# Kernel tuning notes

Measured on AMD Instinct MI355X. Metric: run time of the kernel, lower is better.

Reference implementation:

```python
import jax, jax.numpy as jnp
import numpy as np

N_NODES = 100000

def _sage_conv(x, edge_index, W_l, b_l, W_r):
    # PyG SAGEConv default: mean-aggregate neighbor (source) features at dst,
    # then out = lin_l(agg) + lin_r(x). lin_l has bias, lin_r does not.
    src, dst = edge_index[0], edge_index[1]
    msg = x[src]                                   # [E, F]
    summed = jax.ops.segment_sum(msg, dst, num_segments=N_NODES)  # [N, F]
    cnt = jax.ops.segment_sum(jnp.ones((src.shape[0],), x.dtype), dst,
                              num_segments=N_NODES)
    agg = summed / jnp.maximum(cnt, 1.0)[:, None]
    return agg @ W_l + b_l + x @ W_r


def setup_inputs() -> dict:
    key = jax.random.key(0)
    ks = jax.random.split(key, 10)
    F_IN, H, C = 128, 16, 8
    E = 3200000
    x = jax.random.normal(ks[0], (N_NODES, F_IN), dtype=jnp.float32)
    edge_index = jax.random.randint(ks[1], (2, E), 0, N_NODES, dtype=jnp.int64)
    s1 = 1.0 / np.sqrt(F_IN)
    s2 = 1.0 / np.sqrt(H)
    sc = 1.0 / np.sqrt(2 * H)
    return {
        "x": x,
        "edge_index": edge_index,
        "W1_l": jax.random.uniform(ks[2], (F_IN, H), jnp.float32, -s1, s1),
        "b1": jnp.zeros((H,), jnp.float32),
        "W1_r": jax.random.uniform(ks[3], (F_IN, H), jnp.float32, -s1, s1),
        "W2_l": jax.random.uniform(ks[4], (H, H), jnp.float32, -s2, s2),
        "b2": jnp.zeros((H,), jnp.float32),
        "W2_r": jax.random.uniform(ks[5], (H, H), jnp.float32, -s2, s2),
        "Wc": jax.random.uniform(ks[6], (2 * H, C), jnp.float32, -sc, sc),
        "bc": jax.random.uniform(ks[7], (C,), jnp.float32, -sc, sc),
    }


def reference(x, edge_index, W1_l, b1, W1_r, W2_l, b2, W2_r, Wc, bc):
    h = jax.nn.relu(_sage_conv(x, edge_index, W1_l, b1, W1_r))
    # F.dropout(training=False) in eval mode -> identity
    h = jax.nn.relu(_sage_conv(h, edge_index, W2_l, b2, W2_r))
    edge_feat = jnp.concatenate([h[edge_index[0]], h[edge_index[1]]], axis=-1)  # [E, 32]
    logits = edge_feat @ Wc + bc                                                # [E, C]
    return jax.nn.log_softmax(logits, axis=1)
```

## Files before the change

kernel.cpp:

```cpp
#include <hip/hip_runtime.h>
#include <hip/hip_bf16.h>
#include <hip/hip_fp16.h>


#define NBLK 512
#define BUCKET_BITS 9
#define BUCKET_SZ 512
#define MAXNB 256
#define STAGE_CAP 36000

struct __align__(16) H8 { __half2 a, b, c, d; };

__global__ __launch_bounds__(512) void prep_kernel(const int* __restrict__ ei,
                                                   int* __restrict__ counts,
                                                   const float* __restrict__ x,
                                                   const float* __restrict__ W1l,
                                                   const float* __restrict__ W1r,
                                                   __half* __restrict__ yh,
                                                   float* __restrict__ z,
                                                   int E, int N, int NB, int chunk,
                                                   int nbin) {
  __shared__ float smem[64 * 129 + 128 * 32];
  int t = threadIdx.x;
  if ((int)blockIdx.x < nbin) {
    int* hist = (int*)smem;
    for (int i = t; i < NB; i += 512) hist[i] = 0;
    __syncthreads();
    int s = blockIdx.x * chunk;
    int eend = s + chunk; if (eend > E) eend = E;
    for (int e = s + t; e < eend; e += 512)
      atomicAdd(&hist[ei[E + e] >> BUCKET_BITS], 1);
    __syncthreads();
    for (int b = t; b < NB; b += 512)
      counts[b * NBLK + blockIdx.x] = hist[b];
  } else {
    float* Xs = smem;
    float* Ws = smem + 64 * 129;
    int nb = ((int)blockIdx.x - nbin) * 64;
    for (int i = t; i < 128 * 16; i += 512) {
      int kk = i >> 4, c = i & 15;
      Ws[kk * 32 + c] = W1l[i];
      Ws[kk * 32 + 16 + c] = W1r[i];
    }
    const float4* xg = (const float4*)(x + (size_t)nb * 128);
    for (int i4 = t; i4 < 64 * 32; i4 += 512) {
      int r = i4 >> 5, c4 = (i4 & 31) * 4;
      float4 val = make_float4(0.f, 0.f, 0.f, 0.f);
      if (nb + r < N) val = xg[i4];
      float* dp = &Xs[r * 129 + c4];
      dp[0] = val.x; dp[1] = val.y; dp[2] = val.z; dp[3] = val.w;
    }
    __syncthreads();
    int n = t & 63, cg = t >> 6;
    float a0 = 0.f, a1 = 0.f, a2 = 0.f, a3 = 0.f;
    for (int kk = 0; kk < 128; ++kk) {
      float xv = Xs[n * 129 + kk];
      const float* wr = &Ws[kk * 32 + cg * 4];
      a0 += xv * wr[0]; a1 += xv * wr[1]; a2 += xv * wr[2]; a3 += xv * wr[3];
    }
    int node = nb + n;
    if (node < N) {
      int c = cg * 4;
      if (c < 16) {
        __half2* yp = (__half2*)(yh + (size_t)node * 16 + c);
        yp[0] = __floats2half2_rn(a0, a1);
        yp[1] = __floats2half2_rn(a2, a3);
      } else {
        float* op = z + (size_t)node * 16 + (c - 16);
        op[0] = a0; op[1] = a1; op[2] = a2; op[3] = a3;
      }
    }
  }
}

__global__ __launch_bounds__(512) void scan1_kernel(const int* __restrict__ counts,
                                                    int* __restrict__ locoff,
                                                    int* __restrict__ total) {
  __shared__ int wsum[8];
  int b = blockIdx.x;
  int t = threadIdx.x;
  int lane = t & 63, wid = t >> 6;
  int v = counts[b * NBLK + t];
  int incl = v;
#pragma unroll
  for (int d = 1; d < 64; d <<= 1) {
    int u = __shfl_up(incl, d);
    if (lane >= d) incl += u;
  }
  if (lane == 63) wsum[wid] = incl;
  __syncthreads();
  if (t < 64) {
    int w = (t < 8) ? wsum[t] : 0;
#pragma unroll
    for (int d = 1; d < 8; d <<= 1) {
      int u = __shfl_up(w, d);
      if (lane >= d) w += u;
    }
    if (t < 8) wsum[t] = w;
  }
  __syncthreads();
  int excl = ((wid > 0) ? wsum[wid - 1] : 0) + (incl - v);
  locoff[b * NBLK + t] = excl;
  if (t == NBLK - 1) total[b] = excl + v;
}

__global__ __launch_bounds__(512) void binwrite_kernel(const int* __restrict__ ei,
                                                       const int* __restrict__ locoff,
                                                       const int* __restrict__ total,
                                                       int* __restrict__ elist,
                                                       int E, int NB, int chunk) {
  __shared__ int cur[MAXNB];
  __shared__ int ws4[4];
  int t = threadIdx.x;
  int lane = t & 63, wid = t >> 6;
  int v = (t < 256 && t < NB) ? total[t] : 0;
  int incl = v;
#pragma unroll
  for (int d = 1; d < 64; d <<= 1) {
    int u = __shfl_up(incl, d);
    if (lane >= d) incl += u;
  }
  if (t < 256 && lane == 63) ws4[wid] = incl;
  __syncthreads();
  if (t < 64) {
    int w = (t < 4) ? ws4[t] : 0;
#pragma unroll
    for (int d = 1; d < 4; d <<= 1) {
      int u = __shfl_up(w, d);
      if (lane >= d) w += u;
    }
    if (t < 4) ws4[t] = w;
  }
  __syncthreads();
  if (t < 256 && t < NB)
    cur[t] = ((wid > 0) ? ws4[wid - 1] : 0) + (incl - v) + locoff[t * NBLK + blockIdx.x];
  __syncthreads();
  int s = blockIdx.x * chunk;
  int eend = s + chunk; if (eend > E) eend = E;
  for (int e = s + t; e < eend; e += 512) {
    int src = ei[e];
    int dst = ei[E + e];
    int b = dst >> BUCKET_BITS;
    int pos = atomicAdd(&cur[b], 1);
    elist[pos] = ((dst & (BUCKET_SZ - 1)) << 17) | src;
  }
}

__global__ __launch_bounds__(1024) void sort_kernel(int* __restrict__ elist,
                                                    const int* __restrict__ total,
                                                    int* __restrict__ row_csr,
                                                    int N, int NB) {
  extern __shared__ int sm[];
  int* stage = sm;
  int* hist  = sm + STAGE_CAP;
  int* wtmp  = hist + 512;
  __shared__ int beg_s;
  int t = threadIdx.x;
  int b = blockIdx.x;
  int lane = t & 63, wid = t >> 6;
  {
    int v = (t < 256 && t < NB) ? total[t] : 0;
    int incl = v;
#pragma unroll
    for (int d = 1; d < 64; d <<= 1) {
      int u = __shfl_up(incl, d);
      if (lane >= d) incl += u;
    }
    if (t < 256 && lane == 63) wtmp[wid] = incl;
    __syncthreads();
    if (t < 64) {
      int w = (t < 4) ? wtmp[t] : 0;
#pragma unroll
      for (int d = 1; d < 4; d <<= 1) {
        int u = __shfl_up(w, d);
        if (lane >= d) w += u;
      }
      if (t < 4) wtmp[t] = w;
    }
    __syncthreads();
    if (t == b) beg_s = ((wid > 0) ? wtmp[wid - 1] : 0) + (incl - v);
    __syncthreads();
  }
  int beg = beg_s;
  int cnt = total[b];
  if (cnt > STAGE_CAP) cnt = STAGE_CAP;
  for (int i = t; i < cnt; i += 1024) stage[i] = elist[beg + i];
  if (t < 512) hist[t] = 0;
  __syncthreads();
  for (int i = t; i < cnt; i += 1024)
    atomicAdd(&hist[((unsigned)stage[i]) >> 17], 1);
  __syncthreads();
  int v = (t < 512) ? hist[t] : 0;
  int incl = v;
#pragma unroll
  for (int d = 1; d < 64; d <<= 1) {
    int u = __shfl_up(incl, d);
    if (lane >= d) incl += u;
  }
  if (t < 512 && lane == 63) wtmp[wid] = incl;
  __syncthreads();
  if (t < 64) {
    int w = (t < 8) ? wtmp[t] : 0;
#pragma unroll
    for (int d = 1; d < 8; d <<= 1) {
      int u = __shfl_up(w, d);
      if (lane >= d) w += u;
    }
    if (t < 8) wtmp[t] = w;
  }
  __syncthreads();
  if (t < 512) {
    int excl = ((wid > 0) ? wtmp[wid - 1] : 0) + (incl - v);
    hist[t] = excl;
    int node = (b << BUCKET_BITS) + t;
    if (node <= N) row_csr[node] = beg + excl;
  }
  __syncthreads();
  for (int i = t; i < cnt; i += 1024) {
    unsigned ent = (unsigned)stage[i];
    int pos = atomicAdd(&hist[ent >> 17], 1);
    elist[beg + pos] = ent & 0x1FFFF;
  }
}

__global__ __launch_bounds__(256) void agg1_kernel(const __half* __restrict__ yh,
                                                   const float* __restrict__ z,
                                                   const int* __restrict__ row_csr,
                                                   const int* __restrict__ srclist,
                                                   const float* __restrict__ b1,
                                                   const float* __restrict__ W2l,
                                                   const float* __restrict__ W2r,
                                                   __half* __restrict__ ph,
                                                   float* __restrict__ q, int N) {
  __shared__ float Wl_s[256], Wr_s[256], b_s[16];
  int t = threadIdx.x;
  if (t < 256) { Wl_s[t] = W2l[t]; Wr_s[t] = W2r[t]; }
  if (t < 16) b_s[t] = b1[t];
  __syncthreads();
  int g = (blockIdx.x * 256 + t) >> 3;
  int k = t & 7;
  if (g >= N) return;
  int beg = row_csr[g], end = row_csr[g + 1];
  const __half2* yh2 = (const __half2*)yh;
  float a0 = 0.f, a1 = 0.f;
  int j = beg;
  for (; j + 4 <= end; j += 4) {
    int s0 = srclist[j], s1 = srclist[j + 1];
    int s2 = srclist[j + 2], s3 = srclist[j + 3];
    float2 v0 = __half22float2(yh2[(size_t)s0 * 8 + k]);
    float2 v1 = __half22float2(yh2[(size_t)s1 * 8 + k]);
    float2 v2 = __half22float2(yh2[(size_t)s2 * 8 + k]);
    float2 v3 = __half22float2(yh2[(size_t)s3 * 8 + k]);
    a0 += v0.x + v1.x + v2.x + v3.x;
    a1 += v0.y + v1.y + v2.y + v3.y;
  }
  for (; j < end; ++j) {
    float2 v = __half22float2(yh2[(size_t)srclist[j] * 8 + k]);
    a0 += v.x; a1 += v.y;
  }
  int deg = end - beg;
  float inv = 1.f / (float)(deg > 0 ? deg : 1);
  float2 zv = ((const float2*)z)[(size_t)g * 8 + k];
  float h0 = fmaxf(a0 * inv + b_s[2 * k]     + zv.x, 0.f);
  float h1 = fmaxf(a1 * inv + b_s[2 * k + 1] + zv.y, 0.f);
  float pa0 = 0.f, pa1 = 0.f, qa0 = 0.f, qa1 = 0.f;
  int c0 = 2 * k;
#pragma unroll
  for (int kk2 = 0; kk2 < 8; ++kk2) {
    float ha = __shfl(h0, kk2, 8);
    float hb = __shfl(h1, kk2, 8);
    int r0 = 2 * kk2 * 16, r1 = r0 + 16;
    pa0 += ha * Wl_s[r0 + c0]     + hb * Wl_s[r1 + c0];
    pa1 += ha * Wl_s[r0 + c0 + 1] + hb * Wl_s[r1 + c0 + 1];
    qa0 += ha * Wr_s[r0 + c0]     + hb * Wr_s[r1 + c0];
    qa1 += ha * Wr_s[r0 + c0 + 1] + hb * Wr_s[r1 + c0 + 1];
  }
  ((__half2*)ph)[(size_t)g * 8 + k] = __floats2half2_rn(pa0, pa1);
  ((float2*)q)[(size_t)g * 8 + k] = make_float2(qa0, qa1);
}

__global__ __launch_bounds__(256) void agg2_kernel(const __half* __restrict__ ph,
                                                   const float* __restrict__ q,
                                                   const int* __restrict__ row_csr,
                                                   const int* __restrict__ srclist,
                                                   const float* __restrict__ b2,
                                                   const float* __restrict__ Wc,
                                                   __half* __restrict__ Uh,
                                                   __half* __restrict__ Vh, int N) {
  __shared__ float Wc_s[256], b_s[16];
  int t = threadIdx.x;
  if (t < 256) Wc_s[t] = Wc[t];
  if (t < 16) b_s[t] = b2[t];
  __syncthreads();
  int g = (blockIdx.x * 256 + t) >> 3;
  int k = t & 7;
  if (g >= N) return;
  int beg = row_csr[g], end = row_csr[g + 1];
  const __half2* ph2 = (const __half2*)ph;
  float a0 = 0.f, a1 = 0.f;
  int j = beg;
  for (; j + 4 <= end; j += 4) {
    int s0 = srclist[j], s1 = srclist[j + 1];
    int s2 = srclist[j + 2], s3 = srclist[j + 3];
    float2 v0 = __half22float2(ph2[(size_t)s0 * 8 + k]);
    float2 v1 = __half22float2(ph2[(size_t)s1 * 8 + k]);
    float2 v2 = __half22float2(ph2[(size_t)s2 * 8 + k]);
    float2 v3 = __half22float2(ph2[(size_t)s3 * 8 + k]);
    a0 += v0.x + v1.x + v2.x + v3.x;
    a1 += v0.y + v1.y + v2.y + v3.y;
  }
  for (; j < end; ++j) {
    float2 v = __half22float2(ph2[(size_t)srclist[j] * 8 + k]);
    a0 += v.x; a1 += v.y;
  }
  int deg = end - beg;
  float inv = 1.f / (float)(deg > 0 ? deg : 1);
  float2 qv = ((const float2*)q)[(size_t)g * 8 + k];
  float h0 = fmaxf(a0 * inv + b_s[2 * k]     + qv.x, 0.f);
  float h1 = fmaxf(a1 * inv + b_s[2 * k + 1] + qv.y, 0.f);
  int wb = (k < 4) ? 0 : 128;
  int c0 = 2 * (k & 3);
  float o0 = 0.f, o1 = 0.f;
#pragma unroll
  for (int kk2 = 0; kk2 < 8; ++kk2) {
    float ha = __shfl(h0, kk2, 8);
    float hb = __shfl(h1, kk2, 8);
    int r0 = wb + 2 * kk2 * 8, r1 = r0 + 8;
    o0 += ha * Wc_s[r0 + c0]     + hb * Wc_s[r1 + c0];
    o1 += ha * Wc_s[r0 + c0 + 1] + hb * Wc_s[r1 + c0 + 1];
  }
  __half2 o = __floats2half2_rn(o0, o1);
  if (k < 4) ((__half2*)Uh)[(size_t)g * 4 + k] = o;
  else       ((__half2*)Vh)[(size_t)g * 4 + (k - 4)] = o;
}

__global__ __launch_bounds__(256) void edge_out_kernel(const int* __restrict__ ei,
                                                       const __half* __restrict__ Uh,
                                                       const __half* __restrict__ Vh,
                                                       const float* __restrict__ bc,
                                                       float* __restrict__ out, int E) {
  int base = blockIdx.x * 1024 + threadIdx.x;
  float4 c0 = ((const float4*)bc)[0], c1 = ((const float4*)bc)[1];
  int s[4], d[4];
#pragma unroll
  for (int ii = 0; ii < 4; ++ii) {
    int e = base + ii * 256;
    s[ii] = (e < E) ? ei[e] : 0;
    d[ii] = (e < E) ? ei[E + e] : 0;
  }
  H8 u8[4], v8[4];
#pragma unroll
  for (int ii = 0; ii < 4; ++ii) {
    u8[ii] = *(const H8*)(Uh + (size_t)s[ii] * 8);
    v8[ii] = *(const H8*)(Vh + (size_t)d[ii] * 8);
  }
#pragma unroll
  for (int ii = 0; ii < 4; ++ii) {
    int e = base + ii * 256;
    if (e >= E) continue;
    float2 ua = __half22float2(u8[ii].a), ub = __half22float2(u8[ii].b);
    float2 uc = __half22float2(u8[ii].c), ud = __half22float2(u8[ii].d);
    float2 va = __half22float2(v8[ii].a), vb = __half22float2(v8[ii].b);
    float2 vc = __half22float2(v8[ii].c), vd = __half22float2(v8[ii].d);
    float tv[8];
    tv[0] = ua.x + va.x + c0.x; tv[1] = ua.y + va.y + c0.y;
    tv[2] = ub.x + vb.x + c0.z; tv[3] = ub.y + vb.y + c0.w;
    tv[4] = uc.x + vc.x + c1.x; tv[5] = uc.y + vc.y + c1.y;
    tv[6] = ud.x + vd.x + c1.z; tv[7] = ud.y + vd.y + c1.w;
    float m = tv[0];
#pragma unroll
    for (int c = 1; c < 8; ++c) m = fmaxf(m, tv[c]);
    float ssum = 0.f;
#pragma unroll
    for (int c = 0; c < 8; ++c) ssum += __expf(tv[c] - m);
    float lse = m + __logf(ssum);
    float4 o0 = make_float4(tv[0] - lse, tv[1] - lse, tv[2] - lse, tv[3] - lse);
    float4 o1 = make_float4(tv[4] - lse, tv[5] - lse, tv[6] - lse, tv[7] - lse);
    float4* op = (float4*)(out + (size_t)e * 8);
    op[0] = o0; op[1] = o1;
  }
}

extern "C" void kernel_launch(void* const* d_in, const int* in_sizes, int n_in,
                              void* d_out, int out_size, void* d_ws, size_t ws_size,
                              hipStream_t stream) {
  const float* x   = (const float*)d_in[0];
  const int*   ei  = (const int*)d_in[1];
  const float* W1l = (const float*)d_in[2];
  const float* b1  = (const float*)d_in[3];
  const float* W1r = (const float*)d_in[4];
  const float* W2l = (const float*)d_in[5];
  const float* b2  = (const float*)d_in[6];
  const float* W2r = (const float*)d_in[7];
  const float* Wc  = (const float*)d_in[8];
  const float* bc  = (const float*)d_in[9];
  float* out = (float*)d_out;

  const int N = in_sizes[0] / 128;
  const int E = in_sizes[1] / 2;
  const size_t N16 = (size_t)N * 16;
  const int NB = (N + BUCKET_SZ - 1) >> BUCKET_BITS;
  const int chunk = (E + NBLK - 1) / NBLK;

  __half* yh = (__half*)d_ws;
  __half* ph = yh + N16;
  __half* Uh = ph + N16;
  __half* Vh = Uh + (size_t)N * 8;
  float*  z  = (float*)(Vh + (size_t)N * 8);
  float*  q  = z + N16;
  int* counts  = (int*)(q + N16);
  int* locoff  = counts + NB * NBLK;
  int* total   = locoff + NB * NBLK;
  int* elist   = total + NB;
  int* row_csr = elist + E;

  int lin1_blocks = (N + 63) / 64;
  prep_kernel<<<NBLK + lin1_blocks, 512, 0, stream>>>(ei, counts, x, W1l, W1r,
                                                      yh, z, E, N, NB, chunk, NBLK);
  scan1_kernel<<<NB, 512, 0, stream>>>(counts, locoff, total);
  binwrite_kernel<<<NBLK, 512, 0, stream>>>(ei, locoff, total, elist, E, NB, chunk);
  size_t smem = (STAGE_CAP + 512 + 16) * sizeof(int);
  sort_kernel<<<NB, 1024, smem, stream>>>(elist, total, row_csr, N, NB);

  int ngrid = (N * 8 + 255) / 256;
  agg1_kernel<<<ngrid, 256, 0, stream>>>(yh, z, row_csr, elist, b1, W2l, W2r, ph, q, N);
  agg2_kernel<<<ngrid, 256, 0, stream>>>(ph, q, row_csr, elist, b2, Wc, Uh, Vh, N);

  int egrid = (E + 1023) / 1024;
  edge_out_kernel<<<egrid, 256, 0, stream>>>(ei, Uh, Vh, bc, out, E);
}
```

Baseline: 197.2 us.

## Fuse first-layer aggregation into bucket sort kernel using LDS-resident sorted lists

Merges agg1 into the bucket sort kernel. Each sort block keeps its sorted source list in shared memory and aggregates its 512 destination nodes right away, then applies the second-layer weights. This removes a kernel launch and the global re-read of row_csr and srclist. In exchange, the gather phase runs on only about 196 large blocks instead of thousands of small ones, and shared memory use per block grows. STAGE_CAP is halved so the staging and sorted buffers both fit, and edge_out now uses nontemporal loads for the edge indices.

```diff
diff --git a/kernel.cpp b/kernel.cpp
--- a/kernel.cpp
+++ b/kernel.cpp
@@ -7,7 +7,7 @@
 #define BUCKET_BITS 9
 #define BUCKET_SZ 512
 #define MAXNB 256
-#define STAGE_CAP 36000
+#define STAGE_CAP 18000
 
 struct __align__(16) H8 { __half2 a, b, c, d; };
 
@@ -146,18 +146,31 @@
   }
 }
 
-__global__ __launch_bounds__(1024) void sort_kernel(int* __restrict__ elist,
-                                                    const int* __restrict__ total,
-                                                    int* __restrict__ row_csr,
-                                                    int N, int NB) {
+__global__ __launch_bounds__(1024) void sortagg_kernel(int* __restrict__ elist,
+                                                       const int* __restrict__ total,
+                                                       int* __restrict__ row_csr,
+                                                       const __half* __restrict__ yh,
+                                                       const float* __restrict__ z,
+                                                       const float* __restrict__ b1,
+                                                       const float* __restrict__ W2l,
+                                                       const float* __restrict__ W2r,
+                                                       __half* __restrict__ ph,
+                                                       float* __restrict__ q,
+                                                       int N, int NB) {
   extern __shared__ int sm[];
-  int* stage = sm;
-  int* hist  = sm + STAGE_CAP;
-  int* wtmp  = hist + 512;
+  int* stage  = sm;
+  int* sorted = sm + STAGE_CAP;
+  int* hist   = sm + 2 * STAGE_CAP;
+  int* wtmp   = hist + 512;
+  float* Wl_s = (float*)(wtmp + 16);
+  float* Wr_s = Wl_s + 256;
+  float* b_s  = Wr_s + 256;
   __shared__ int beg_s;
   int t = threadIdx.x;
   int b = blockIdx.x;
   int lane = t & 63, wid = t >> 6;
+  if (t < 256) { Wl_s[t] = W2l[t]; Wr_s[t] = W2r[t]; }
+  else if (t < 272) b_s[t - 256] = b1[t - 256];
   {
     int v = (t < 256 && t < NB) ? total[t] : 0;
     int incl = v;
@@ -190,93 +203,89 @@
   for (int i = t; i < cnt; i += 1024)
     atomicAdd(&hist[((unsigned)stage[i]) >> 17], 1);
   __syncthreads();
-  int v = (t < 512) ? hist[t] : 0;
-  int incl = v;
-#pragma unroll
-  for (int d = 1; d < 64; d <<= 1) {
-    int u = __shfl_up(incl, d);
-    if (lane >= d) incl += u;
-  }
-  if (t < 512 && lane == 63) wtmp[wid] = incl;
-  __syncthreads();
-  if (t < 64) {
-    int w = (t < 8) ? wtmp[t] : 0;
-#pragma unroll
-    for (int d = 1; d < 8; d <<= 1) {
-      int u = __shfl_up(w, d);
-      if (lane >= d) w += u;
-    }
-    if (t < 8) wtmp[t] = w;
-  }
-  __syncthreads();
-  if (t < 512) {
-    int excl = ((wid > 0) ? wtmp[wid - 1] : 0) + (incl - v);
-    hist[t] = excl;
-    int node = (b << BUCKET_BITS) + t;
-    if (node <= N) row_csr[node] = beg + excl;
+  {
+    int v = (t < 512) ? hist[t] : 0;
+    int incl = v;
+#pragma unroll
+    for (int d = 1; d < 64; d <<= 1) {
+      int u = __shfl_up(incl, d);
+      if (lane >= d) incl += u;
+    }
+    if (t < 512 && lane == 63) wtmp[wid] = incl;
+    __syncthreads();
+    if (t < 64) {
+      int w = (t < 8) ? wtmp[t] : 0;
+#pragma unroll
+      for (int d = 1; d < 8; d <<= 1) {
+        int u = __shfl_up(w, d);
+        if (lane >= d) w += u;
+      }
+      if (t < 8) wtmp[t] = w;
+    }
+    __syncthreads();
+    if (t < 512) {
+      int excl = ((wid > 0) ? wtmp[wid - 1] : 0) + (incl - v);
+      hist[t] = excl;
+      int node = (b << BUCKET_BITS) + t;
+      if (node <= N) row_csr[node] = beg + excl;
+    }
   }
   __syncthreads();
   for (int i = t; i < cnt; i += 1024) {
     unsigned ent = (unsigned)stage[i];
     int pos = atomicAdd(&hist[ent >> 17], 1);
-    elist[beg + pos] = ent & 0x1FFFF;
-  }
-}
-
-__global__ __launch_bounds__(256) void agg1_kernel(const __half* __restrict__ yh,
-                                                   const float* __restrict__ z,
-                                                   const int* __restrict__ row_csr,
-                                                   const int* __restrict__ srclist,
-                                                   const float* __restrict__ b1,
-                                                   const float* __restrict__ W2l,
-                                                   const float* __restrict__ W2r,
-                                                   __half* __restrict__ ph,
-                                                   float* __restrict__ q, int N) {
-  __shared__ float Wl_s[256], Wr_s[256], b_s[16];
-  int t = threadIdx.x;
-  if (t < 256) { Wl_s[t] = W2l[t]; Wr_s[t] = W2r[t]; }
-  if (t < 16) b_s[t] = b1[t];
-  __syncthreads();
-  int g = (blockIdx.x * 256 + t) >> 3;
+    int src = ent & 0x1FFFF;
+    sorted[pos] = src;
+    elist[beg + pos] = src;
+  }
+  __syncthreads();
+  const __half2* yh2 = (const __half2*)yh;
+  int base = b << BUCKET_BITS;
   int k = t & 7;
-  if (g >= N) return;
-  int beg = row_csr[g], end = row_csr[g + 1];
-  const __half2* yh2 = (const __half2*)yh;
-  float a0 = 0.f, a1 = 0.f;
-  int j = beg;
-  for (; j + 4 <= end; j += 4) {
-    int s0 = srclist[j], s1 = srclist[j + 1];
-    int s2 = srclist[j + 2], s3 = srclist[j + 3];
-    float2 v0 = __half22float2(yh2[(size_t)s0 * 8 + k]);
-    float2 v1 = __half22float2(yh2[(size_t)s1 * 8 + k]);
-    float2 v2 = __half22float2(yh2[(size_t)s2 * 8 + k]);
-    float2 v3 = __half22float2(yh2[(size_t)s3 * 8 + k]);
-    a0 += v0.x + v1.x + v2.x + v3.x;
-    a1 += v0.y + v1.y + v2.y + v3.y;
-  }
-  for (; j < end; ++j) {
-    float2 v = __half22float2(yh2[(size_t)srclist[j] * 8 + k]);
-    a0 += v.x; a1 += v.y;
-  }
-  int deg = end - beg;
-  float inv = 1.f / (float)(deg > 0 ? deg : 1);
-  float2 zv = ((const float2*)z)[(size_t)g * 8 + k];
-  float h0 = fmaxf(a0 * inv + b_s[2 * k]     + zv.x, 0.f);
-  float h1 = fmaxf(a1 * inv + b_s[2 * k + 1] + zv.y, 0.f);
-  float pa0 = 0.f, pa1 = 0.f, qa0 = 0.f, qa1 = 0.f;
-  int c0 = 2 * k;
-#pragma unroll
-  for (int kk2 = 0; kk2 < 8; ++kk2) {
-    float ha = __shfl(h0, kk2, 8);
-    float hb = __shfl(h1, kk2, 8);
-    int r0 = 2 * kk2 * 16, r1 = r0 + 16;
-    pa0 += ha * Wl_s[r0 + c0]     + hb * Wl_s[r1 + c0];
-    pa1 += ha * Wl_s[r0 + c0 + 1] + hb * Wl_s[r1 + c0 + 1];
-    qa0 += ha * Wr_s[r0 + c0]     + hb * Wr_s[r1 + c0];
-    qa1 += ha * Wr_s[r0 + c0 + 1] + hb * Wr_s[r1 + c0 + 1];
-  }
-  ((__half2*)ph)[(size_t)g * 8 + k] = __floats2half2_rn(pa0, pa1);
-  ((float2*)q)[(size_t)g * 8 + k] = make_float2(qa0, qa1);
+#pragma unroll
+  for (int pass = 0; pass < 4; ++pass) {
+    int dl = pass * 128 + (t >> 3);
+    int node = base + dl;
+    if (node < N) {
+      int rbeg = dl ? hist[dl - 1] : 0;
+      int rend = hist[dl];
+      float a0 = 0.f, a1 = 0.f;
+      int j = rbeg;
+      for (; j + 4 <= rend; j += 4) {
+        int s0 = sorted[j], s1 = sorted[j + 1];
+        int s2 = sorted[j + 2], s3 = sorted[j + 3];
+        float2 v0 = __half22float2(yh2[(size_t)s0 * 8 + k]);
+        float2 v1 = __half22float2(yh2[(size_t)s1 * 8 + k]);
+        float2 v2 = __half22float2(yh2[(size_t)s2 * 8 + k]);
+        float2 v3 = __half22float2(yh2[(size_t)s3 * 8 + k]);
+        a0 += v0.x + v1.x + v2.x + v3.x;
+        a1 += v0.y + v1.y + v2.y + v3.y;
+      }
+      for (; j < rend; ++j) {
+        float2 v = __half22float2(yh2[(size_t)sorted[j] * 8 + k]);
+        a0 += v.x; a1 += v.y;
+      }
+      int deg = rend - rbeg;
+      float inv = 1.f / (float)(deg > 0 ? deg : 1);
+      float2 zv = ((const float2*)z)[(size_t)node * 8 + k];
+      float h0 = fmaxf(a0 * inv + b_s[2 * k]     + zv.x, 0.f);
+      float h1 = fmaxf(a1 * inv + b_s[2 * k + 1] + zv.y, 0.f);
+      float pa0 = 0.f, pa1 = 0.f, qa0 = 0.f, qa1 = 0.f;
+      int c0 = 2 * k;
+#pragma unroll
+      for (int kk2 = 0; kk2 < 8; ++kk2) {
+        float ha = __shfl(h0, kk2, 8);
+        float hb = __shfl(h1, kk2, 8);
+        int r0 = 2 * kk2 * 16, r1 = r0 + 16;
+        pa0 += ha * Wl_s[r0 + c0]     + hb * Wl_s[r1 + c0];
+        pa1 += ha * Wl_s[r0 + c0 + 1] + hb * Wl_s[r1 + c0 + 1];
+        qa0 += ha * Wr_s[r0 + c0]     + hb * Wr_s[r1 + c0];
+        qa1 += ha * Wr_s[r0 + c0 + 1] + hb * Wr_s[r1 + c0 + 1];
+      }
+      ((__half2*)ph)[(size_t)node * 8 + k] = __floats2half2_rn(pa0, pa1);
+      ((float2*)q)[(size_t)node * 8 + k] = make_float2(qa0, qa1);
+    }
+  }
 }
 
 __global__ __launch_bounds__(256) void agg2_kernel(const __half* __restrict__ ph,
@@ -345,8 +354,8 @@
 #pragma unroll
   for (int ii = 0; ii < 4; ++ii) {
     int e = base + ii * 256;
-    s[ii] = (e < E) ? ei[e] : 0;
-    d[ii] = (e < E) ? ei[E + e] : 0;
+    s[ii] = (e < E) ? __builtin_nontemporal_load(ei + e) : 0;
+    d[ii] = (e < E) ? __builtin_nontemporal_load(ei + E + e) : 0;
   }
   H8 u8[4], v8[4];
 #pragma unroll
@@ -419,11 +428,12 @@
                                                       yh, z, E, N, NB, chunk, NBLK);
   scan1_kernel<<<NB, 512, 0, stream>>>(counts, locoff, total);
   binwrite_kernel<<<NBLK, 512, 0, stream>>>(ei, locoff, total, elist, E, NB, chunk);
-  size_t smem = (STAGE_CAP + 512 + 16) * sizeof(int);
-  sort_kernel<<<NB, 1024, smem, stream>>>(elist, total, row_csr, N, NB);
+
+  size_t smem = (2 * STAGE_CAP + 512 + 16) * sizeof(int) + 528 * sizeof(float);
+  sortagg_kernel<<<NB, 1024, smem, stream>>>(elist, total, row_csr, yh, z, b1,
+                                             W2l, W2r, ph, q, N, NB);
 
   int ngrid = (N * 8 + 255) / 256;
-  agg1_kernel<<<ngrid, 256, 0, stream>>>(yh, z, row_csr, elist, b1, W2l, W2r, ph, q, N);
   agg2_kernel<<<ngrid, 256, 0, stream>>>(ph, q, row_csr, elist, b2, Wc, Uh, Vh, N);
 
   int egrid = (E + 1023) / 1024;
```

After: 208.2 us. 5.6% more time.
